# Optimization experiments

Hardware: AMD Instinct MI355X
Metric: run time of the kernel (lower is better)

The kernel has to match this reference:

```python
import jax, jax.numpy as jnp
import numpy as np

B, S, D, H = 2, 2048, 1024, 16
DK = D // H


def setup_inputs() -> dict:
    key = jax.random.key(0)
    ks = jax.random.split(key, 11)
    scale = jnp.float32(1.0 / np.sqrt(D))
    inp = {
        "query": jax.random.normal(ks[0], (B, S, D), jnp.float32),
        "key": jax.random.normal(ks[1], (B, S, D), jnp.float32),
        "value": jax.random.normal(ks[2], (B, S, D), jnp.float32),
        # causal mask: True = masked (masked_fill semantics), broadcast over batch/heads
        "mask": jnp.triu(jnp.ones((S, S), dtype=bool), k=1)[None, None, :, :],
        "Wq": jax.random.normal(ks[3], (D, D), jnp.float32) * scale,
        "bq": jnp.zeros((D,), jnp.float32),
        "Wk": jax.random.normal(ks[4], (D, D), jnp.float32) * scale,
        "bk": jnp.zeros((D,), jnp.float32),
        "Wv": jax.random.normal(ks[5], (D, D), jnp.float32) * scale,
        "bv": jnp.zeros((D,), jnp.float32),
        "Wo": jax.random.normal(ks[6], (D, D), jnp.float32) * scale,
        "bo": jnp.zeros((D,), jnp.float32),
    }
    return inp


def _split_heads(x):
    # (B, S, D) -> (B, H, S, DK)
    b, s, _ = x.shape
    return x.reshape(b, s, H, DK).transpose(0, 2, 1, 3)


def reference(query, key, value, mask, Wq, bq, Wk, bk, Wv, bv, Wo, bo):
    # nn.Linear: y = x @ W.T + b
    q = _split_heads(query @ Wq.T + bq)
    k = _split_heads(key @ Wk.T + bk)
    v = _split_heads(value @ Wv.T + bv)

    inv_sqrt_dk = jnp.float32(1.0 / np.sqrt(DK))
    scores = jnp.einsum("bhqd,bhkd->bhqk", q, k) * inv_sqrt_dk  # (B,H,S,S)
    scores = jnp.where(mask, jnp.float32(-jnp.inf), scores)
    weights = jax.nn.softmax(scores, axis=-1)
    weights = jnp.nan_to_num(weights, nan=0.0)  # fully-masked rows -> 0

    attn = jnp.einsum("bhqk,bhkd->bhqd", weights, v)  # (B,H,S,DK)
    merged = attn.transpose(0, 2, 1, 3).reshape(B, S, D)  # merge heads
    return merged @ Wo.T + bo
```

## Files before the change

kernel.cpp:

```cpp
#include <hip/hip_runtime.h>


typedef unsigned short u16;
typedef unsigned int u32;
typedef __attribute__((ext_vector_type(8))) __bf16 bf16x8;
typedef __attribute__((ext_vector_type(8))) unsigned short us8;
typedef __attribute__((ext_vector_type(4))) float f32x4;

#define S_LEN 2048
#define D_DIM 1024
#define NH 16
#define DKH 64
#define Mi 1048576ULL

__device__ __forceinline__ u16 f2bf(float f) {
  return __builtin_bit_cast(u16, (__bf16)f);
}
__device__ __forceinline__ bf16x8 ld_frag(const u16* p) {
  us8 v = *(const us8*)p;
  return __builtin_bit_cast(bf16x8, v);
}
__device__ __forceinline__ void gl2lds16(const u16* g, u16* l) {
  __builtin_amdgcn_global_load_lds(
      (__attribute__((address_space(1))) void*)(g),
      (__attribute__((address_space(3))) void*)(l), 16, 0, 0);
}

__global__ __launch_bounds__(256, 1) void cvt_all(
    const float* __restrict__ q, const float* __restrict__ k, const float* __restrict__ v,
    const float* __restrict__ wq, const float* __restrict__ wk,
    const float* __restrict__ wv, const float* __restrict__ wo,
    u16* __restrict__ dst)
{
  size_t e0 = ((size_t)blockIdx.x * 256 + threadIdx.x) * 8;
  const float* s;
  if      (e0 <  4*Mi) s = q  + e0;
  else if (e0 <  8*Mi) s = k  + (e0 - 4*Mi);
  else if (e0 < 12*Mi) s = v  + (e0 - 8*Mi);
  else if (e0 < 13*Mi) s = wq + (e0 - 12*Mi);
  else if (e0 < 14*Mi) s = wk + (e0 - 13*Mi);
  else if (e0 < 15*Mi) s = wv + (e0 - 14*Mi);
  else                 s = wo + (e0 - 15*Mi);
  float4 a = ((const float4*)s)[0];
  float4 b = ((const float4*)s)[1];
  us8 o;
  o[0]=f2bf(a.x); o[1]=f2bf(a.y); o[2]=f2bf(a.z); o[3]=f2bf(a.w);
  o[4]=f2bf(b.x); o[5]=f2bf(b.y); o[6]=f2bf(b.z); o[7]=f2bf(b.w);
  *(us8*)(dst + e0) = o;
}

__global__ __launch_bounds__(256, 1) void gemm_qkv_bb(
    const u16* __restrict__ Aq, const u16* __restrict__ Ak, const u16* __restrict__ Av,
    const u16* __restrict__ Wqb, const u16* __restrict__ Wkb, const u16* __restrict__ Wvb,
    const float* __restrict__ bq, const float* __restrict__ bk, const float* __restrict__ bv,
    u16* __restrict__ Oq, u16* __restrict__ Ok, u16* __restrict__ Ov, float qscale)
{
  const int z = blockIdx.z;
  const u16* A = (z == 0) ? Aq : (z == 1) ? Ak : Av;
  const u16* W = (z == 0) ? Wqb : (z == 1) ? Wkb : Wvb;
  const float* bias = (z == 0) ? bq : (z == 1) ? bk : bv;
  u16* out = (z == 0) ? Oq : (z == 1) ? Ok : Ov;
  const float scale = (z == 0) ? qscale : 1.0f;
  const int K = 1024;

  __shared__ u16 lA[128 * 32];
  __shared__ u16 lB[128 * 32];
  const int t = threadIdx.x;
  const int w = t >> 6, l = t & 63;
  const int mblk = blockIdx.y * 128, nblk = blockIdx.x * 128;
  const int wm = (w & 1) * 64, wn = (w >> 1) * 64;
  const int lr = l & 15, lq = l >> 4;
  const int srow = l >> 2, scol = (l & 3) * 8;

  f32x4 acc[4][4] = {};

  for (int k0 = 0; k0 < K; k0 += 32) {
    __syncthreads();
    #pragma unroll
    for (int r = 0; r < 2; ++r) {
      int grp = r * 4 + w;
      gl2lds16(A + (size_t)(mblk + grp * 16 + srow) * K + k0 + scol, &lA[grp * 512]);
      gl2lds16(W + (size_t)(nblk + grp * 16 + srow) * K + k0 + scol, &lB[grp * 512]);
    }
    __syncthreads();
    bf16x8 aF[4], bF[4];
    #pragma unroll
    for (int mt = 0; mt < 4; ++mt)
      aF[mt] = ld_frag(&lA[(wm + mt * 16 + lr) * 32 + lq * 8]);
    #pragma unroll
    for (int nt = 0; nt < 4; ++nt)
      bF[nt] = ld_frag(&lB[(wn + nt * 16 + lr) * 32 + lq * 8]);
    #pragma unroll
    for (int mt = 0; mt < 4; ++mt)
      #pragma unroll
      for (int nt = 0; nt < 4; ++nt)
        acc[mt][nt] = __builtin_amdgcn_mfma_f32_16x16x32_bf16(aF[mt], bF[nt], acc[mt][nt], 0, 0, 0);
  }

  #pragma unroll
  for (int mt = 0; mt < 4; ++mt)
    #pragma unroll
    for (int nt = 0; nt < 4; ++nt)
      #pragma unroll
      for (int r = 0; r < 4; ++r) {
        int rowg = mblk + wm + mt * 16 + lq * 4 + r;
        int colg = nblk + wn + nt * 16 + lr;
        float v = (acc[mt][nt][r] + bias[colg]) * scale;
        int b = rowg >> 11, s = rowg & 2047;
        int h = colg >> 6, dk = colg & 63;
        if (z != 2)
          out[(((size_t)(b * NH + h)) * S_LEN + s) * DKH + dk] = f2bf(v);
        else
          out[(((size_t)(b * NH + h)) * DKH + dk) * S_LEN + s] = f2bf(v);
      }
}

__global__ __launch_bounds__(256, 1) void gemm_out_bb(
    const u16* __restrict__ A, const u16* __restrict__ W,
    const float* __restrict__ bias, float* __restrict__ out)
{
  const int K = 1024;
  __shared__ u16 lA[128 * 64];
  __shared__ u16 lB[64 * 64];
  const int bid = blockIdx.x;
  const int o   = (bid & 7) * 64 + (bid >> 3);
  const int mblk = (o >> 4) * 128, nblk = (o & 15) * 64;
  const int t = threadIdx.x;
  const int w = t >> 6, l = t & 63;
  const int wm = (w & 1) * 64, wn = (w >> 1) * 32;
  const int lr = l & 15, lq = l >> 4;
  const int srow = l >> 3;
  const int sgr  = (l & 7) ^ srow;

  f32x4 acc[4][2] = {};

  for (int k0 = 0; k0 < K; k0 += 64) {
    __syncthreads();
    #pragma unroll
    for (int i = 0; i < 4; ++i) {
      int chunk = w * 4 + i;
      int row = chunk * 8 + srow;
      gl2lds16(A + (size_t)(mblk + row) * K + k0 + sgr * 8, &lA[chunk * 512]);
    }
    #pragma unroll
    for (int i = 0; i < 2; ++i) {
      int chunk = w * 2 + i;
      int row = chunk * 8 + srow;
      gl2lds16(W + (size_t)(nblk + row) * K + k0 + sgr * 8, &lB[chunk * 512]);
    }
    __syncthreads();
    #pragma unroll
    for (int kk = 0; kk < 2; ++kk) {
      bf16x8 aF[4], bF[2];
      #pragma unroll
      for (int mt = 0; mt < 4; ++mt)
        aF[mt] = ld_frag(&lA[(wm + mt * 16 + lr) * 64 + ((kk * 4 + lq) ^ (lr & 7)) * 8]);
      #pragma unroll
      for (int nt = 0; nt < 2; ++nt)
        bF[nt] = ld_frag(&lB[(wn + nt * 16 + lr) * 64 + ((kk * 4 + lq) ^ (lr & 7)) * 8]);
      #pragma unroll
      for (int mt = 0; mt < 4; ++mt)
        #pragma unroll
        for (int nt = 0; nt < 2; ++nt)
          acc[mt][nt] = __builtin_amdgcn_mfma_f32_16x16x32_bf16(aF[mt], bF[nt], acc[mt][nt], 0, 0, 0);
    }
  }

  #pragma unroll
  for (int mt = 0; mt < 4; ++mt)
    #pragma unroll
    for (int nt = 0; nt < 2; ++nt)
      #pragma unroll
      for (int r = 0; r < 4; ++r) {
        int rowg = mblk + wm + mt * 16 + lq * 4 + r;
        int colg = nblk + wn + nt * 16 + lr;
        out[(size_t)rowg * D_DIM + colg] = acc[mt][nt][r] + bias[colg];
      }
}

__global__ __launch_bounds__(256, 1) void attn_fused(
    const u16* __restrict__ Q, const u16* __restrict__ K,
    const u16* __restrict__ Vt, u16* __restrict__ O)
{
  __shared__ u16 lK[2][64 * 64];
  __shared__ u16 lV[2][64 * 64];

  const int idx = blockIdx.x;
  const int o   = (idx & 7) * 128 + (idx >> 3);
  const int bh  = (o >> 7) * 4 + (o & 3);
  const int ts  = (o >> 2) & 31;
  const int qt  = (ts & 1) ? (31 - (ts >> 1)) : (ts >> 1);
  const int b = bh >> 4, h = bh & 15;
  const int t = threadIdx.x;
  const int w = t >> 6, l = t & 63;
  const int lr = l & 15, lq = l >> 4;

  const u16* Qp = Q + (size_t)bh * S_LEN * DKH;
  const u16* Kp = K + (size_t)bh * S_LEN * DKH;
  const u16* Vp = Vt + (size_t)bh * DKH * S_LEN;

  const int srow8 = l >> 3;
  const int schunk = l & 7;

  const int qrow = qt * 64 + w * 16 + lr;
  bf16x8 qf[2];
  qf[0] = ld_frag(Qp + (size_t)qrow * DKH + lq * 8);
  qf[1] = ld_frag(Qp + (size_t)qrow * DKH + 32 + lq * 8);

  f32x4 o4[4] = {};
  f32x4 li4 = {};

  #pragma unroll
  for (int r2 = 0; r2 < 2; ++r2) {
    int grp = r2 * 4 + w;
    int row = grp * 8 + srow8;
    int sw = (row & 3) | (((row >> 3) & 1) << 2);
    int c = schunk ^ sw;
    gl2lds16(Kp + (size_t)row * DKH + c * 8, &lK[0][grp * 512]);
    gl2lds16(Vp + (size_t)row * S_LEN + c * 8, &lV[0][grp * 512]);
  }

  for (int kt = 0; kt <= qt; ++kt) {
    const int cur = kt & 1;
    __syncthreads();

    if (kt < qt) {
      #pragma unroll
      for (int r2 = 0; r2 < 2; ++r2) {
        int grp = r2 * 4 + w;
        int row = grp * 8 + srow8;
        int sw = (row & 3) | (((row >> 3) & 1) << 2);
        int c = schunk ^ sw;
        gl2lds16(Kp + (size_t)((kt + 1) * 64 + row) * DKH + c * 8, &lK[cur ^ 1][grp * 512]);
        gl2lds16(Vp + (size_t)row * S_LEN + (kt + 1) * 64 + c * 8, &lV[cur ^ 1][grp * 512]);
      }
    }

    f32x4 st[4] = {};
    #pragma unroll
    for (int ksd = 0; ksd < 2; ++ksd)
      #pragma unroll
      for (int nt = 0; nt < 4; ++nt) {
        int sig = 32 * (nt >> 1) + 8 * (lr >> 2) + 4 * (nt & 1) + (lr & 3);
        int slot = (ksd * 4 + lq) ^ (lr & 7);
        bf16x8 kb = ld_frag(&lK[cur][sig * 64 + slot * 8]);
        st[nt] = __builtin_amdgcn_mfma_f32_16x16x32_bf16(kb, qf[ksd], st[nt], 0, 0, 0);
      }

    float p[4][4];
    const bool diag = (kt == qt);
    const int qloc = w * 16 + lr;
    #pragma unroll
    for (int nt = 0; nt < 4; ++nt)
      #pragma unroll
      for (int r = 0; r < 4; ++r) {
        int kk = 32 * (nt >> 1) + 8 * lq + 4 * (nt & 1) + r;
        float e = exp2f(st[nt][r]);
        p[nt][r] = (diag && kk > qloc) ? 0.0f : e;
        li4[r] += p[nt][r];
      }

    #pragma unroll
    for (int ks = 0; ks < 2; ++ks) {
      us8 av;
      #pragma unroll
      for (int j = 0; j < 4; ++j) {
        av[j] = f2bf(p[2 * ks][j]);
        av[4 + j] = f2bf(p[2 * ks + 1][j]);
      }
      bf16x8 pa = __builtin_bit_cast(bf16x8, av);
      #pragma unroll
      for (int dblk = 0; dblk < 4; ++dblk) {
        int d = dblk * 16 + lr;
        int sw = (d & 3) | (((d >> 3) & 1) << 2);
        int slot = (4 * ks + lq) ^ sw;
        bf16x8 vb = ld_frag(&lV[cur][d * 64 + slot * 8]);
        o4[dblk] = __builtin_amdgcn_mfma_f32_16x16x32_bf16(pa, vb, o4[dblk], 0, 0, 0);
      }
    }
  }

  float li = li4[0] + li4[1] + li4[2] + li4[3];
  li += __shfl_xor(li, 16);
  li += __shfl_xor(li, 32);
  float ri[4];
  #pragma unroll
  for (int r = 0; r < 4; ++r) ri[r] = 1.0f / __shfl(li, lq * 4 + r);

  const size_t obase = ((size_t)b * S_LEN + qt * 64 + w * 16) * D_DIM + h * DKH;
  #pragma unroll
  for (int dblk = 0; dblk < 4; ++dblk)
    #pragma unroll
    for (int r = 0; r < 4; ++r)
      O[obase + (size_t)(lq * 4 + r) * D_DIM + dblk * 16 + lr] = f2bf(o4[dblk][r] * ri[r]);
}

extern "C" void kernel_launch(void* const* d_in, const int* in_sizes, int n_in,
                              void* d_out, int out_size, void* d_ws, size_t ws_size,
                              hipStream_t stream) {
  const float* query = (const float*)d_in[0];
  const float* key   = (const float*)d_in[1];
  const float* value = (const float*)d_in[2];
  const float* Wq = (const float*)d_in[4];
  const float* bq = (const float*)d_in[5];
  const float* Wk = (const float*)d_in[6];
  const float* bk = (const float*)d_in[7];
  const float* Wv = (const float*)d_in[8];
  const float* bv = (const float*)d_in[9];
  const float* Wo = (const float*)d_in[10];
  const float* bo = (const float*)d_in[11];
  float* out = (float*)d_out;

  const float qscale = 0.125f * 1.44269504088896341f;
  dim3 blk(256);

  u16* base = (u16*)d_ws;
  u16* Qb = base;
  u16* Kb = base + 4 * Mi;
  u16* Vb = base + 8 * Mi;

  u16* cvt = base + 12 * Mi;
  u16* qbf = cvt;
  u16* kbf = cvt + 4 * Mi;
  u16* vbf = cvt + 8 * Mi;
  u16* wqb = cvt + 12 * Mi;
  u16* wkb = cvt + 13 * Mi;
  u16* wvb = cvt + 14 * Mi;
  u16* wob = cvt + 15 * Mi;
  u16* Ab  = qbf;

  cvt_all<<<dim3(8192), blk, 0, stream>>>(query, key, value, Wq, Wk, Wv, Wo, cvt);
  gemm_qkv_bb<<<dim3(8, 32, 3), blk, 0, stream>>>(qbf, kbf, vbf, wqb, wkb, wvb,
                                                  bq, bk, bv, Qb, Kb, Vb, qscale);
  attn_fused<<<dim3(1024), blk, 0, stream>>>(Qb, Kb, Vb, Ab);
  gemm_out_bb<<<dim3(512), blk, 0, stream>>>(Ab, wob, bo, out);
}
```

Measured before the change: 235.3 us.

## Use persistent attention blocks with atomic work queue, longest tiles first

The attention kernel becomes persistent: 768 blocks take (q-tile, head) items from a global atomic counter, starting with the longest causal rows, so load balances dynamically. The counter lives in the output buffer and is zeroed by the convert kernel; the output GEMM overwrites it later. The diagonal tile is peeled out of the loop so off-diagonal tiles skip the mask check, and exp2f is replaced by a raw v_exp_f32. The costs are an atomic plus two barriers per item and reliance on launch ordering to reset the counter.

```diff
diff --git a/kernel.cpp b/kernel.cpp
--- a/kernel.cpp
+++ b/kernel.cpp
@@ -20,6 +20,11 @@
   us8 v = *(const us8*)p;
   return __builtin_bit_cast(bf16x8, v);
 }
+__device__ __forceinline__ float fast_exp2(float x) {
+  float r;
+  asm("v_exp_f32 %0, %1" : "=v"(r) : "v"(x));
+  return r;
+}
 __device__ __forceinline__ void gl2lds16(const u16* g, u16* l) {
   __builtin_amdgcn_global_load_lds(
       (__attribute__((address_space(1))) void*)(g),
@@ -30,8 +35,9 @@
     const float* __restrict__ q, const float* __restrict__ k, const float* __restrict__ v,
     const float* __restrict__ wq, const float* __restrict__ wk,
     const float* __restrict__ wv, const float* __restrict__ wo,
-    u16* __restrict__ dst)
+    u16* __restrict__ dst, u32* __restrict__ cnt)
 {
+  if (blockIdx.x == 0 && threadIdx.x == 0) *cnt = 0;
   size_t e0 = ((size_t)blockIdx.x * 256 + threadIdx.x) * 8;
   const float* s;
   if      (e0 <  4*Mi) s = q  + e0;
@@ -180,119 +186,161 @@
 
 __global__ __launch_bounds__(256, 1) void attn_fused(
     const u16* __restrict__ Q, const u16* __restrict__ K,
-    const u16* __restrict__ Vt, u16* __restrict__ O)
+    const u16* __restrict__ Vt, u16* __restrict__ O, u32* __restrict__ cnt)
 {
   __shared__ u16 lK[2][64 * 64];
   __shared__ u16 lV[2][64 * 64];
-
-  const int idx = blockIdx.x;
-  const int o   = (idx & 7) * 128 + (idx >> 3);
-  const int bh  = (o >> 7) * 4 + (o & 3);
-  const int ts  = (o >> 2) & 31;
-  const int qt  = (ts & 1) ? (31 - (ts >> 1)) : (ts >> 1);
-  const int b = bh >> 4, h = bh & 15;
+  __shared__ int s_item;
+
   const int t = threadIdx.x;
   const int w = t >> 6, l = t & 63;
   const int lr = l & 15, lq = l >> 4;
-
-  const u16* Qp = Q + (size_t)bh * S_LEN * DKH;
-  const u16* Kp = K + (size_t)bh * S_LEN * DKH;
-  const u16* Vp = Vt + (size_t)bh * DKH * S_LEN;
-
   const int srow8 = l >> 3;
   const int schunk = l & 7;
 
-  const int qrow = qt * 64 + w * 16 + lr;
-  bf16x8 qf[2];
-  qf[0] = ld_frag(Qp + (size_t)qrow * DKH + lq * 8);
-  qf[1] = ld_frag(Qp + (size_t)qrow * DKH + 32 + lq * 8);
-
-  f32x4 o4[4] = {};
-  f32x4 li4 = {};
-
-  #pragma unroll
-  for (int r2 = 0; r2 < 2; ++r2) {
-    int grp = r2 * 4 + w;
-    int row = grp * 8 + srow8;
-    int sw = (row & 3) | (((row >> 3) & 1) << 2);
-    int c = schunk ^ sw;
-    gl2lds16(Kp + (size_t)row * DKH + c * 8, &lK[0][grp * 512]);
-    gl2lds16(Vp + (size_t)row * S_LEN + c * 8, &lV[0][grp * 512]);
+  #define STAGE(T, bsel)                                                          \
+    do {                                                                          \
+      _Pragma("unroll")                                                           \
+      for (int r2 = 0; r2 < 2; ++r2) {                                            \
+        int grp = r2 * 4 + w;                                                     \
+        int row = grp * 8 + srow8;                                                \
+        int sw = (row & 3) | (((row >> 3) & 1) << 2);                             \
+        int c = schunk ^ sw;                                                      \
+        gl2lds16(Kp + (size_t)((T) * 64 + row) * DKH + c * 8, &lK[bsel][grp * 512]); \
+        gl2lds16(Vp + (size_t)row * S_LEN + (T) * 64 + c * 8, &lV[bsel][grp * 512]); \
+      }                                                                           \
+    } while (0)
+
+  while (true) {
+    __syncthreads();
+    if (t == 0) s_item = (int)atomicAdd(cnt, 1u);
+    __syncthreads();
+    const int item = s_item;
+    if (item >= 1024) break;
+    const int qt = 31 - (item >> 5);
+    const int bh = item & 31;
+    const int b = bh >> 4, h = bh & 15;
+
+    const u16* Qp = Q + (size_t)bh * S_LEN * DKH;
+    const u16* Kp = K + (size_t)bh * S_LEN * DKH;
+    const u16* Vp = Vt + (size_t)bh * DKH * S_LEN;
+
+    const int qrow = qt * 64 + w * 16 + lr;
+    bf16x8 qf[2];
+    qf[0] = ld_frag(Qp + (size_t)qrow * DKH + lq * 8);
+    qf[1] = ld_frag(Qp + (size_t)qrow * DKH + 32 + lq * 8);
+
+    f32x4 o4[4] = {};
+    f32x4 li4 = {};
+
+    STAGE(0, 0);
+
+    for (int kt = 0; kt < qt; ++kt) {
+      const int cur = kt & 1;
+      __syncthreads();
+      STAGE(kt + 1, cur ^ 1);
+
+      f32x4 st[4] = {};
+      #pragma unroll
+      for (int ksd = 0; ksd < 2; ++ksd)
+        #pragma unroll
+        for (int nt = 0; nt < 4; ++nt) {
+          int sig = 32 * (nt >> 1) + 8 * (lr >> 2) + 4 * (nt & 1) + (lr & 3);
+          int slot = (ksd * 4 + lq) ^ (lr & 7);
+          bf16x8 kb = ld_frag(&lK[cur][sig * 64 + slot * 8]);
+          st[nt] = __builtin_amdgcn_mfma_f32_16x16x32_bf16(kb, qf[ksd], st[nt], 0, 0, 0);
+        }
+
+      float p[4][4];
+      #pragma unroll
+      for (int nt = 0; nt < 4; ++nt)
+        #pragma unroll
+        for (int r = 0; r < 4; ++r) {
+          p[nt][r] = fast_exp2(st[nt][r]);
+          li4[r] += p[nt][r];
+        }
+
+      #pragma unroll
+      for (int ks = 0; ks < 2; ++ks) {
+        us8 av;
+        #pragma unroll
+        for (int j = 0; j < 4; ++j) {
+          av[j] = f2bf(p[2 * ks][j]);
+          av[4 + j] = f2bf(p[2 * ks + 1][j]);
+        }
+        bf16x8 pa = __builtin_bit_cast(bf16x8, av);
+        #pragma unroll
+        for (int dblk = 0; dblk < 4; ++dblk) {
+          int d = dblk * 16 + lr;
+          int sw = (d & 3) | (((d >> 3) & 1) << 2);
+          int slot = (4 * ks + lq) ^ sw;
+          bf16x8 vb = ld_frag(&lV[cur][d * 64 + slot * 8]);
+          o4[dblk] = __builtin_amdgcn_mfma_f32_16x16x32_bf16(pa, vb, o4[dblk], 0, 0, 0);
+        }
+      }
+    }
+
+    {
+      const int cur = qt & 1;
+      __syncthreads();
+      f32x4 st[4] = {};
+      #pragma unroll
+      for (int ksd = 0; ksd < 2; ++ksd)
+        #pragma unroll
+        for (int nt = 0; nt < 4; ++nt) {
+          int sig = 32 * (nt >> 1) + 8 * (lr >> 2) + 4 * (nt & 1) + (lr & 3);
+          int slot = (ksd * 4 + lq) ^ (lr & 7);
+          bf16x8 kb = ld_frag(&lK[cur][sig * 64 + slot * 8]);
+          st[nt] = __builtin_amdgcn_mfma_f32_16x16x32_bf16(kb, qf[ksd], st[nt], 0, 0, 0);
+        }
+
+      float p[4][4];
+      const int qloc = w * 16 + lr;
+      #pragma unroll
+      for (int nt = 0; nt < 4; ++nt)
+        #pragma unroll
+        for (int r = 0; r < 4; ++r) {
+          int kk = 32 * (nt >> 1) + 8 * lq + 4 * (nt & 1) + r;
+          float e = fast_exp2(st[nt][r]);
+          p[nt][r] = (kk > qloc) ? 0.0f : e;
+          li4[r] += p[nt][r];
+        }
+
+      #pragma unroll
+      for (int ks = 0; ks < 2; ++ks) {
+        us8 av;
+        #pragma unroll
+        for (int j = 0; j < 4; ++j) {
+          av[j] = f2bf(p[2 * ks][j]);
+          av[4 + j] = f2bf(p[2 * ks + 1][j]);
+        }
+        bf16x8 pa = __builtin_bit_cast(bf16x8, av);
+        #pragma unroll
+        for (int dblk = 0; dblk < 4; ++dblk) {
+          int d = dblk * 16 + lr;
+          int sw = (d & 3) | (((d >> 3) & 1) << 2);
+          int slot = (4 * ks + lq) ^ sw;
+          bf16x8 vb = ld_frag(&lV[cur][d * 64 + slot * 8]);
+          o4[dblk] = __builtin_amdgcn_mfma_f32_16x16x32_bf16(pa, vb, o4[dblk], 0, 0, 0);
+        }
+      }
+    }
+
+    float li = li4[0] + li4[1] + li4[2] + li4[3];
+    li += __shfl_xor(li, 16);
+    li += __shfl_xor(li, 32);
+    float ri[4];
+    #pragma unroll
+    for (int r = 0; r < 4; ++r) ri[r] = 1.0f / __shfl(li, lq * 4 + r);
+
+    const size_t obase = ((size_t)b * S_LEN + qt * 64 + w * 16) * D_DIM + h * DKH;
+    #pragma unroll
+    for (int dblk = 0; dblk < 4; ++dblk)
+      #pragma unroll
+      for (int r = 0; r < 4; ++r)
+        O[obase + (size_t)(lq * 4 + r) * D_DIM + dblk * 16 + lr] = f2bf(o4[dblk][r] * ri[r]);
   }
-
-  for (int kt = 0; kt <= qt; ++kt) {
-    const int cur = kt & 1;
-    __syncthreads();
-
-    if (kt < qt) {
-      #pragma unroll
-      for (int r2 = 0; r2 < 2; ++r2) {
-        int grp = r2 * 4 + w;
-        int row = grp * 8 + srow8;
-        int sw = (row & 3) | (((row >> 3) & 1) << 2);
-        int c = schunk ^ sw;
-        gl2lds16(Kp + (size_t)((kt + 1) * 64 + row) * DKH + c * 8, &lK[cur ^ 1][grp * 512]);
-        gl2lds16(Vp + (size_t)row * S_LEN + (kt + 1) * 64 + c * 8, &lV[cur ^ 1][grp * 512]);
-      }
-    }
-
-    f32x4 st[4] = {};
-    #pragma unroll
-    for (int ksd = 0; ksd < 2; ++ksd)
-      #pragma unroll
-      for (int nt = 0; nt < 4; ++nt) {
-        int sig = 32 * (nt >> 1) + 8 * (lr >> 2) + 4 * (nt & 1) + (lr & 3);
-        int slot = (ksd * 4 + lq) ^ (lr & 7);
-        bf16x8 kb = ld_frag(&lK[cur][sig * 64 + slot * 8]);
-        st[nt] = __builtin_amdgcn_mfma_f32_16x16x32_bf16(kb, qf[ksd], st[nt], 0, 0, 0);
-      }
-
-    float p[4][4];
-    const bool diag = (kt == qt);
-    const int qloc = w * 16 + lr;
-    #pragma unroll
-    for (int nt = 0; nt < 4; ++nt)
-      #pragma unroll
-      for (int r = 0; r < 4; ++r) {
-        int kk = 32 * (nt >> 1) + 8 * lq + 4 * (nt & 1) + r;
-        float e = exp2f(st[nt][r]);
-        p[nt][r] = (diag && kk > qloc) ? 0.0f : e;
-        li4[r] += p[nt][r];
-      }
-
-    #pragma unroll
-    for (int ks = 0; ks < 2; ++ks) {
-      us8 av;
-      #pragma unroll
-      for (int j = 0; j < 4; ++j) {
-        av[j] = f2bf(p[2 * ks][j]);
-        av[4 + j] = f2bf(p[2 * ks + 1][j]);
-      }
-      bf16x8 pa = __builtin_bit_cast(bf16x8, av);
-      #pragma unroll
-      for (int dblk = 0; dblk < 4; ++dblk) {
-        int d = dblk * 16 + lr;
-        int sw = (d & 3) | (((d >> 3) & 1) << 2);
-        int slot = (4 * ks + lq) ^ sw;
-        bf16x8 vb = ld_frag(&lV[cur][d * 64 + slot * 8]);
-        o4[dblk] = __builtin_amdgcn_mfma_f32_16x16x32_bf16(pa, vb, o4[dblk], 0, 0, 0);
-      }
-    }
-  }
-
-  float li = li4[0] + li4[1] + li4[2] + li4[3];
-  li += __shfl_xor(li, 16);
-  li += __shfl_xor(li, 32);
-  float ri[4];
-  #pragma unroll
-  for (int r = 0; r < 4; ++r) ri[r] = 1.0f / __shfl(li, lq * 4 + r);
-
-  const size_t obase = ((size_t)b * S_LEN + qt * 64 + w * 16) * D_DIM + h * DKH;
-  #pragma unroll
-  for (int dblk = 0; dblk < 4; ++dblk)
-    #pragma unroll
-    for (int r = 0; r < 4; ++r)
-      O[obase + (size_t)(lq * 4 + r) * D_DIM + dblk * 16 + lr] = f2bf(o4[dblk][r] * ri[r]);
+  #undef STAGE
 }
 
 extern "C" void kernel_launch(void* const* d_in, const int* in_sizes, int n_in,
@@ -329,9 +377,11 @@
   u16* wob = cvt + 15 * Mi;
   u16* Ab  = qbf;
 
-  cvt_all<<<dim3(8192), blk, 0, stream>>>(query, key, value, Wq, Wk, Wv, Wo, cvt);
+  u32* cnt = (u32*)d_out;
+
+  cvt_all<<<dim3(8192), blk, 0, stream>>>(query, key, value, Wq, Wk, Wv, Wo, cvt, cnt);
   gemm_qkv_bb<<<dim3(8, 32, 3), blk, 0, stream>>>(qbf, kbf, vbf, wqb, wkb, wvb,
                                                   bq, bk, bv, Qb, Kb, Vb, qscale);
-  attn_fused<<<dim3(1024), blk, 0, stream>>>(Qb, Kb, Vb, Ab);
+  attn_fused<<<dim3(768), blk, 0, stream>>>(Qb, Kb, Vb, Ab, cnt);
   gemm_out_bb<<<dim3(512), blk, 0, stream>>>(Ab, wob, bo, out);
 }
```

Result: no change. 231.7 us (-1.5%).
